# Kernel optimization log

Hardware: AMD Instinct MI355X
Metric: run time of the kernel (lower is better)

Reference implementation:

```python
import jax, jax.numpy as jnp
import numpy as np

N_NODES = 50000
N_EDGES = 800000
IN_C, HID_C, OUT_C = 256, 256, 128


def gcn_conv(x, W, b, row, col, n_nodes):
    """PyG GCNConv: linear transform, symmetric-normalized aggregation, bias.
    row/col already include self-loops. Messages flow row -> col."""
    h = x @ W  # [N, out]
    deg = jax.ops.segment_sum(jnp.ones_like(col, dtype=h.dtype), col, num_segments=n_nodes)
    d_inv_sqrt = jnp.where(deg > 0, jax.lax.rsqrt(jnp.maximum(deg, 1e-12)), 0.0)
    norm = d_inv_sqrt[row] * d_inv_sqrt[col]  # [E]
    msg = h[row] * norm[:, None]              # gather + scale, [E, out]
    out = jax.ops.segment_sum(msg, col, num_segments=n_nodes)  # scatter-add
    return out + b


def setup_inputs() -> dict:
    key = jax.random.key(0)
    k_x, k_e, k_w1, k_w2 = jax.random.split(key, 4)
    x = jax.random.normal(k_x, (N_NODES, IN_C), dtype=jnp.float32)
    edge_index = jax.random.randint(k_e, (2, N_EDGES), 0, N_NODES, dtype=jnp.int64)
    # Glorot-style init for GCN weights, zeros bias (PyG default)
    s1 = float(np.sqrt(6.0 / (IN_C + HID_C)))
    s2 = float(np.sqrt(6.0 / (HID_C + OUT_C)))
    W1 = jax.random.uniform(k_w1, (IN_C, HID_C), dtype=jnp.float32, minval=-s1, maxval=s1)
    b1 = jnp.zeros((HID_C,), dtype=jnp.float32)
    W2 = jax.random.uniform(k_w2, (HID_C, OUT_C), dtype=jnp.float32, minval=-s2, maxval=s2)
    b2 = jnp.zeros((OUT_C,), dtype=jnp.float32)
    return {"x": x, "edge_index": edge_index, "W1": W1, "b1": b1, "W2": W2, "b2": b2}


def reference(x, edge_index, W1, b1, W2, b2):
    n = x.shape[0]
    # add self-loops (PyG GCNConv default add_self_loops=True)
    loops = jnp.arange(n, dtype=edge_index.dtype)
    row = jnp.concatenate([edge_index[0], loops])
    col = jnp.concatenate([edge_index[1], loops])
    h = gcn_conv(x, W1, b1, row, col, n)
    h = jax.nn.relu(h)  # dropout p=0.0 -> identity
    out = gcn_conv(h, W2, b2, row, col, n)
    return out
```

## Files before the change

### kernel.cpp

```cpp
#include <hip/hip_runtime.h>

#define NN 50000
#define NE 800000
#define IN_C 256
#define HID_C 256
#define OUT_C 128

#define NET (NE + NN)
#define NBUCK 196
#define CHUNK 4096
#define NPA 196
#define CAP_B 5120
#define NGRP (NN / 16)

typedef unsigned short u16;
typedef unsigned int u32;
typedef __attribute__((ext_vector_type(8))) short short8;
typedef __attribute__((ext_vector_type(4))) short short4_t;
typedef __attribute__((ext_vector_type(8))) unsigned short ushort8;
typedef __attribute__((ext_vector_type(4))) float f32x4;
typedef __attribute__((ext_vector_type(4))) unsigned u32x4;
typedef __attribute__((ext_vector_type(4), aligned(4))) unsigned u32x4u;

#define CPS ((size_t)(NN + 1) * 32)

__device__ __forceinline__ u16 f2b(float f) {
  unsigned int u = __float_as_uint(f);
  return (u16)((u + 0x7FFFu + ((u >> 16) & 1u)) >> 16);
}
__device__ __forceinline__ float b2f(u16 s) {
  return __uint_as_float(((unsigned int)s) << 16);
}


__global__ __launch_bounds__(256) void convw_zero(const float* __restrict__ W1,
                                                  const float* __restrict__ W2,
                                                  u16* __restrict__ W1t,
                                                  u16* __restrict__ W2t,
                                                  int* __restrict__ cnt,
                                                  u16* __restrict__ Hb,
                                                  int nzb) {
  int b = blockIdx.x;
  if (b < 256) {
    int id = b * 256 + threadIdx.x;
    if (id < 256 * 256) {
      int n = id >> 8, k = id & 255;
      W1t[id] = f2b(W1[k * 256 + n]);
    }
    if (id < 128 * 256) {
      int n = id >> 8, k = id & 255;
      W2t[id] = f2b(W2[k * 128 + n]);
    }
  } else if (b < 256 + nzb) {
    int i = (b - 256) * 256 + threadIdx.x;
    if (i < NN) cnt[i] = 1;
  } else {
    int t = threadIdx.x;
    Hb[(size_t)(t >> 5) * CPS + (size_t)NN * 32 + (t & 31)] = 0;
  }
}


__global__ __launch_bounds__(256) void hist_kernel(const int* __restrict__ col,
                                                   int* __restrict__ cnt, int E) {
  int e = blockIdx.x * blockDim.x + threadIdx.x;
  if (e < E) atomicAdd(&cnt[col[e]], 1);
}

__global__ __launch_bounds__(256) void scan1_kernel(const int* __restrict__ cnt,
                                                    int* __restrict__ bsum, int n) {
  __shared__ int ws[4];
  int i = blockIdx.x * 256 + threadIdx.x;
  int lane = threadIdx.x & 63, wid = threadIdx.x >> 6;
  int v = (i < n) ? cnt[i] : 0;
#pragma unroll
  for (int off = 32; off > 0; off >>= 1) v += __shfl_down(v, off, 64);
  if (lane == 0) ws[wid] = v;
  __syncthreads();
  if (threadIdx.x == 0) bsum[blockIdx.x] = ws[0] + ws[1] + ws[2] + ws[3];
}

__global__ __launch_bounds__(256) void scan2_kernel(const int* __restrict__ bsum,
                                                    int* __restrict__ boff,
                                                    int* __restrict__ row_off,
                                                    int nb, int n) {
  __shared__ int wsum[4], wpre[5];
  int lane = threadIdx.x & 63, wid = threadIdx.x >> 6;
  int v = (threadIdx.x < nb) ? bsum[threadIdx.x] : 0;
  int s = v;
#pragma unroll
  for (int off = 1; off < 64; off <<= 1) {
    int t = __shfl_up(s, off, 64);
    if (lane >= off) s += t;
  }
  if (lane == 63) wsum[wid] = s;
  __syncthreads();
  if (threadIdx.x == 0) {
    int acc = 0;
#pragma unroll
    for (int w = 0; w < 4; ++w) { wpre[w] = acc; acc += wsum[w]; }
    wpre[4] = acc;
  }
  __syncthreads();
  if (threadIdx.x < nb) boff[threadIdx.x] = wpre[wid] + (s - v);
  if (threadIdx.x == 0) row_off[n] = wpre[4];
}

__global__ __launch_bounds__(256) void scan3_kernel(const int* __restrict__ cnt,
                                                    const int* __restrict__ boff,
                                                    int* __restrict__ row_off,
                                                    int* __restrict__ bcur,
                                                    float* __restrict__ dinv, int n) {
  __shared__ int wsum[4], wpre[4];
  int i = blockIdx.x * 256 + threadIdx.x;
  int lane = threadIdx.x & 63, wid = threadIdx.x >> 6;
  int v = (i < n) ? cnt[i] : 0;
  int s = v;
#pragma unroll
  for (int off = 1; off < 64; off <<= 1) {
    int t = __shfl_up(s, off, 64);
    if (lane >= off) s += t;
  }
  if (lane == 63) wsum[wid] = s;
  __syncthreads();
  if (threadIdx.x == 0) {
    int acc = 0;
#pragma unroll
    for (int w = 0; w < 4; ++w) { wpre[w] = acc; acc += wsum[w]; }
  }
  __syncthreads();
  if (i < n) {
    int off = boff[blockIdx.x] + wpre[wid] + (s - v);
    row_off[i] = off;
    if ((i & 255) == 0) bcur[i >> 8] = off;
    dinv[i] = rsqrtf((float)v);
  }
}


template <bool A_IS_F32, bool PLANAR_C>
__device__ __forceinline__ void gemm_body(const void* __restrict__ Ap,
                                          const u16* __restrict__ Bt,
                                          const float* __restrict__ dscale,
                                          u16* __restrict__ C, int M, int N,
                                          int bx, int by,
                                          u16 (&Asl)[2][5120], u16 (&Bsl)[2][5120]) {
  const int tid = threadIdx.x;
  const int row0 = by * 128;
  const int col0 = bx * 128;

  f32x4 acc[4][4] = {};

  const int seg = tid & 7;
  const int rb = tid >> 3;
  const int wave = tid >> 6, lane = tid & 63;
  const int wm = wave >> 1, wn = wave & 1;
  const int qr = lane & 15, quad = lane >> 4;

  float4 aF[4];
  ushort4 aU[4];
  ushort4 bR[4];

  auto load_tiles = [&](int k0) {
    if constexpr (A_IS_F32) {
      const float* A = (const float*)Ap;
#pragma unroll
      for (int i = 0; i < 4; ++i) {
        int gr = row0 + rb + i * 32;
        aF[i] = (gr < M) ? *(const float4*)&A[(size_t)gr * 256 + k0 + seg * 4]
                         : make_float4(0.f, 0.f, 0.f, 0.f);
      }
    } else {
      const u16* A = (const u16*)Ap;
#pragma unroll
      for (int i = 0; i < 4; ++i) {
        int gr = row0 + rb + i * 32;
        aU[i] = (gr < M) ? *(const ushort4*)&A[(size_t)gr * 256 + k0 + seg * 4]
                         : make_ushort4(0, 0, 0, 0);
      }
    }
#pragma unroll
    for (int i = 0; i < 4; ++i) {
      int n = rb + i * 32;
      bR[i] = *(const ushort4*)&Bt[(size_t)(col0 + n) * 256 + k0 + seg * 4];
    }
  };

  auto write_lds = [&](int buf) {
#pragma unroll
    for (int i = 0; i < 4; ++i) {
      int r = rb + i * 32;
      ushort4 u;
      if constexpr (A_IS_F32) {
        u.x = f2b(aF[i].x); u.y = f2b(aF[i].y);
        u.z = f2b(aF[i].z); u.w = f2b(aF[i].w);
      } else {
        u = aU[i];
      }
      *(ushort4*)&Asl[buf][r * 40 + seg * 4] = u;
      *(ushort4*)&Bsl[buf][r * 40 + seg * 4] = bR[i];
    }
  };

  load_tiles(0);
  write_lds(0);
  __syncthreads();

#pragma unroll
  for (int it = 0; it < 8; ++it) {
    const int cur = it & 1;
    if (it < 7) load_tiles((it + 1) * 32);

    short8 afr[4], bfr[4];
#pragma unroll
    for (int mt = 0; mt < 4; ++mt)
      afr[mt] = *(const short8*)&Asl[cur][(wm * 64 + mt * 16 + qr) * 40 + quad * 8];
#pragma unroll
    for (int nt = 0; nt < 4; ++nt)
      bfr[nt] = *(const short8*)&Bsl[cur][(wn * 64 + nt * 16 + qr) * 40 + quad * 8];
#pragma unroll
    for (int mt = 0; mt < 4; ++mt)
#pragma unroll
      for (int nt = 0; nt < 4; ++nt)
        acc[mt][nt] = __builtin_amdgcn_mfma_f32_16x16x32_bf16(afr[mt], bfr[nt], acc[mt][nt], 0, 0, 0);

    if (it < 7) {
      write_lds(1 - cur);
      __syncthreads();
    }
  }

#pragma unroll
  for (int mt = 0; mt < 4; ++mt) {
#pragma unroll
    for (int i = 0; i < 4; ++i) {
      int gr = row0 + wm * 64 + mt * 16 + quad * 4 + i;
      if (gr < M) {
        float sc = dscale[gr];
#pragma unroll
        for (int nt = 0; nt < 4; ++nt) {
          int gc = col0 + wn * 64 + nt * 16 + qr;
          u16 val = f2b(acc[mt][nt][i] * sc);
          if constexpr (PLANAR_C)
            C[(size_t)(gc >> 5) * CPS + (size_t)gr * 32 + (gc & 31)] = val;
          else
            C[(size_t)gr * N + gc] = val;
        }
      }
    }
  }
}

template <bool A_IS_F32, bool PLANAR_C>
__global__ __launch_bounds__(256) void gemm_mfma(const void* __restrict__ Ap,
                                                 const u16* __restrict__ Bt,
                                                 const float* __restrict__ dscale,
                                                 u16* __restrict__ C, int M, int N,
                                                 u16* __restrict__ zrow) {
  if (zrow != nullptr && blockIdx.x == 0 && blockIdx.y == 0 && threadIdx.x < 128) {
    int t = threadIdx.x;
    zrow[(size_t)(t >> 5) * CPS + (size_t)NN * 32 + (t & 31)] = 0;
  }
  __shared__ u16 Asl[2][5120];
  __shared__ u16 Bsl[2][5120];
  gemm_body<A_IS_F32, PLANAR_C>(Ap, Bt, dscale, C, M, N, blockIdx.x, blockIdx.y, Asl, Bsl);
}

__global__ __launch_bounds__(256) void gemm1_scatter(const float* __restrict__ x,
                                                     const u16* __restrict__ W1t,
                                                     const float* __restrict__ dinv,
                                                     u16* __restrict__ Hb, int M, int N,
                                                     int ngb,
                                                     const int* __restrict__ row,
                                                     const int* __restrict__ col,
                                                     int* __restrict__ bcur,
                                                     uint2* __restrict__ stage, int E) {
  __shared__ u16 ABsl[4][5120];
  int b = blockIdx.x;
  if (b < ngb) {
    gemm_body<true, true>(x, W1t, dinv, Hb, M, N, b & 1, b >> 1,
                          *reinterpret_cast<u16(*)[2][5120]>(&ABsl[0]),
                          *reinterpret_cast<u16(*)[2][5120]>(&ABsl[2]));
  } else {
    uint2* pairs = (uint2*)ABsl;
    int* hcnt = (int*)((char*)ABsl + 32768);
    int* hscan = hcnt + 256;
    int* hbase = hscan + 256;
    int* lcur = hbase + 256;

    const int tid = threadIdx.x;
    const int blk = b - ngb;
    const int e0 = blk * CHUNK;

    hcnt[tid] = 0;
    __syncthreads();

    int ecol[16], erow[16];
#pragma unroll
    for (int j = 0; j < 16; ++j) {
      int e = e0 + j * 256 + tid;
      if (e < E) {
        ecol[j] = col[e];
        erow[j] = row[e];
        atomicAdd(&hcnt[ecol[j] >> 8], 1);
      } else {
        ecol[j] = -1;
      }
    }
    __syncthreads();

    hscan[tid] = hcnt[tid];
    __syncthreads();
#pragma unroll
    for (int off = 1; off < 256; off <<= 1) {
      int t = (tid >= off) ? hscan[tid - off] : 0;
      __syncthreads();
      hscan[tid] += t;
      __syncthreads();
    }

    lcur[tid] = 0;
    if (hcnt[tid] > 0) hbase[tid] = atomicAdd(&bcur[tid], hcnt[tid]);
    __syncthreads();

#pragma unroll
    for (int j = 0; j < 16; ++j) {
      if (ecol[j] >= 0) {
        int bk = ecol[j] >> 8;
        int p = atomicAdd(&lcur[bk], 1);
        pairs[(hscan[bk] - hcnt[bk]) + p] = make_uint2((unsigned)erow[j], (unsigned)ecol[j]);
      }
    }
    __syncthreads();

    int mtot = hscan[255];
    for (int s = tid; s < mtot; s += 256) {
      uint2 pr = pairs[s];
      int bk = (int)(pr.y >> 8);
      stage[hbase[bk] + (s - (hscan[bk] - hcnt[bk]))] = pr;
    }
  }
}

__global__ __launch_bounds__(256) void csr_sort(const uint2* __restrict__ stage,
                                                const int* __restrict__ row_off,
                                                u32* __restrict__ csrp) {
  __shared__ int cur[256];
  __shared__ u32 outb[CAP_B];
  const int b = blockIdx.x;
  const int base_node = b << 8;
  const int nnodes = min(256, NN - base_node);
  const int tid = threadIdx.x;
  const int bstart = row_off[base_node];
  const int bend = row_off[min(base_node + 256, NN)];
  if (tid < nnodes) {
    int c0 = row_off[base_node + tid] - bstart;
    outb[c0] = (u32)(base_node + tid) | ((u32)(tid & 15) << 16);
    cur[tid] = c0 + 1;
  }
  __syncthreads();
  const int m = bend - bstart;
  const int mreal = m - nnodes;
  for (int i = tid; i < mreal; i += 256) {
    uint2 pr = stage[bstart + i];
    int cl = ((int)pr.y - base_node) & 255;
    int p = atomicAdd(&cur[cl], 1);
    u32 val = (pr.x & 0xFFFFu) | ((u32)(cl & 15) << 16);
    if (p < CAP_B) outb[p] = val;
    else if (bstart + p < NET) csrp[bstart + p] = val;
  }
  __syncthreads();
  const int mm = min(m, CAP_B);
  for (int i = tid; i < mm; i += 256) csrp[bstart + i] = outb[i];
}

template <int NPL, int OUTC, bool RELU_BF16>
__global__ __launch_bounds__(256) void agg_mfma(const u16* __restrict__ h,
                                                const int* __restrict__ row_off,
                                                const u32* __restrict__ csrp,
                                                const float* __restrict__ dinv,
                                                const float* __restrict__ bias,
                                                void* __restrict__ outp) {
  __shared__ char lds[4][2048];
  const int slice = blockIdx.x % NPL;
  const int wave = threadIdx.x >> 6;
  const int g = (blockIdx.x / NPL) * 4 + wave;
  if (g >= NGRP) return;
  const int lane = threadIdx.x & 63;
  const int qr = lane & 15, quad = lane >> 4;
  const int s = lane >> 1, half = lane & 1;
  const u16* hpl = h + (size_t)slice * CPS;
  const int beg = row_off[g * 16];
  const int end = row_off[g * 16 + 16];
  char* wl = lds[wave];
  char* wp = wl + (half * 1024 + ((s >> 2) & 1) * 512 + (s >> 3) * 128 + (s & 3) * 32);
  const unsigned trb = (unsigned)(size_t)(wl) + (unsigned)(lane * 8);

  f32x4 acc0 = {}, acc1 = {};
  for (int base = beg; base < end; base += 32) {
    int p = base + s;
    unsigned src = (p < end) ? (csrp[p] & 0xFFFFu) : (unsigned)NN;
    const u16* rp = hpl + (size_t)src * 32 + half * 16;
    u32x4 d0 = *(const u32x4*)rp;
    u32x4 d1 = *(const u32x4*)(rp + 8);
    u32x4u w0 = *(const u32x4u*)&csrp[base + quad * 8];
    u32x4u w1 = *(const u32x4u*)&csrp[base + quad * 8 + 4];
    short8 afr;
#pragma unroll
    for (int j = 0; j < 4; ++j) {
      afr[j]     = (short)(((w0[j] >> 16) == (unsigned)qr) ? 0x3F80 : 0);
      afr[j + 4] = (short)(((w1[j] >> 16) == (unsigned)qr) ? 0x3F80 : 0);
    }
    *(u32x4*)wp = d0;
    *(u32x4*)(wp + 16) = d1;
    short4_t t00, t01, t10, t11;
    asm volatile("s_waitcnt lgkmcnt(0)\n\t"
                 "ds_read_b64_tr_b16 %0, %4 offset:0\n\t"
                 "ds_read_b64_tr_b16 %1, %4 offset:512\n\t"
                 "ds_read_b64_tr_b16 %2, %4 offset:1024\n\t"
                 "ds_read_b64_tr_b16 %3, %4 offset:1536\n\t"
                 "s_waitcnt lgkmcnt(0)"
                 : "=&v"(t00), "=&v"(t01), "=&v"(t10), "=&v"(t11)
                 : "v"(trb)
                 : "memory");
    __builtin_amdgcn_sched_barrier(0);
    short8 b0 = __builtin_shufflevector(t00, t01, 0, 1, 2, 3, 4, 5, 6, 7);
    short8 b1 = __builtin_shufflevector(t10, t11, 0, 1, 2, 3, 4, 5, 6, 7);
    acc0 = __builtin_amdgcn_mfma_f32_16x16x32_bf16(afr, b0, acc0, 0, 0, 0);
    acc1 = __builtin_amdgcn_mfma_f32_16x16x32_bf16(afr, b1, acc1, 0, 0, 0);
  }
  const int node0 = g * 16 + quad * 4;
  const int chb = slice * 32;
  float bv0 = bias[chb + qr];
  float bv1 = bias[chb + 16 + qr];
#pragma unroll
  for (int i = 0; i < 4; ++i) {
    float dv = dinv[node0 + i];
    float r0 = acc0[i] * dv + bv0;
    float r1 = acc1[i] * dv + bv1;
    if constexpr (RELU_BF16) {
      u16* o = (u16*)outp;
      o[(size_t)(node0 + i) * OUTC + chb + qr] = f2b(fmaxf(r0, 0.f));
      o[(size_t)(node0 + i) * OUTC + chb + 16 + qr] = f2b(fmaxf(r1, 0.f));
    } else {
      float* o = (float*)outp;
      o[(size_t)(node0 + i) * OUTC + chb + qr] = r0;
      o[(size_t)(node0 + i) * OUTC + chb + 16 + qr] = r1;
    }
  }
}


extern "C" void kernel_launch(void* const* d_in, const int* in_sizes, int n_in,
                              void* d_out, int out_size, void* d_ws, size_t ws_size,
                              hipStream_t stream) {
  const float* x = (const float*)d_in[0];
  const int* ei = (const int*)d_in[1];
  const float* W1 = (const float*)d_in[2];
  const float* b1 = (const float*)d_in[3];
  const float* W2 = (const float*)d_in[4];
  const float* b2 = (const float*)d_in[5];
  float* out = (float*)d_out;

  const int* row = ei;
  const int* col = ei + NE;

  const int NB = (NN + 255) / 256;

  u16* Hb = (u16*)d_ws;
  u16* H2b = Hb + (size_t)(NN + 1) * 256;
  u16* H3b = H2b + (size_t)NN * 256;
  u16* W1t = H3b + (size_t)(NN + 1) * 128;
  u16* W2t = W1t + 256 * 256;
  int* cnt = (int*)(W2t + 128 * 256);
  int* row_off = cnt + NN;
  int* bcur = row_off + NN + 4;
  float* dinv = (float*)(bcur + 256);
  int* bsum = (int*)(dinv + NN);
  int* boff = bsum + 200;
  u32* csrp = (u32*)(boff + 200);
  uint2* stage = (uint2*)H3b;

  convw_zero<<<256 + NB + 1, 256, 0, stream>>>(W1, W2, W1t, W2t, cnt, Hb, NB);
  hist_kernel<<<(NE + 255) / 256, 256, 0, stream>>>(col, cnt, NE);
  scan1_kernel<<<NB, 256, 0, stream>>>(cnt, bsum, NN);
  scan2_kernel<<<1, 256, 0, stream>>>(bsum, boff, row_off, NB, NN);
  scan3_kernel<<<NB, 256, 0, stream>>>(cnt, boff, row_off, bcur, dinv, NN);

  {
    const int ngb = (HID_C / 128) * ((NN + 127) / 128);
    gemm1_scatter<<<ngb + NPA, 256, 0, stream>>>(x, W1t, dinv, Hb, NN, HID_C, ngb,
                                                 row, col, bcur, stage, NE);
  }
  csr_sort<<<NBUCK, 256, 0, stream>>>(stage, row_off, csrp);

  const int NG4 = (NGRP + 3) / 4;
  agg_mfma<8, 256, true><<<NG4 * 8, 256, 0, stream>>>(
      Hb, row_off, csrp, dinv, b1, H2b);

  {
    dim3 grid(OUT_C / 128, (NN + 127) / 128);
    gemm_mfma<false, true><<<grid, 256, 0, stream>>>(H2b, W2t, dinv, H3b, NN, OUT_C, H3b);
  }

  agg_mfma<4, 128, false><<<NG4 * 4, 256, 0, stream>>>(
      H3b, row_off, csrp, dinv, b2, out);
}
```

Baseline: 277.9 us.

## Software-pipeline CSR index and feature gathers in MFMA aggregation loop

After: 328.8 us. 1.18x slower.

```diff
diff --git a/kernel.cpp b/kernel.cpp
--- a/kernel.cpp
+++ b/kernel.cpp
@@ -392,27 +392,41 @@
   const u16* hpl = h + (size_t)slice * CPS;
   const int beg = row_off[g * 16];
   const int end = row_off[g * 16 + 16];
+  const int nsteps = (end - beg + 31) >> 5;
   char* wl = lds[wave];
   char* wp = wl + (half * 1024 + ((s >> 2) & 1) * 512 + (s >> 3) * 128 + (s & 3) * 32);
   const unsigned trb = (unsigned)(size_t)(wl) + (unsigned)(lane * 8);
 
+  auto ldC = [&](int t, u32& cw, u32x4u& w0, u32x4u& w1) {
+    int base = beg + t * 32;
+    cw = __builtin_nontemporal_load(&csrp[base + s]);
+    w0 = __builtin_nontemporal_load((const u32x4u*)&csrp[base + quad * 8]);
+    w1 = __builtin_nontemporal_load((const u32x4u*)&csrp[base + quad * 8 + 4]);
+  };
+  auto ldG = [&](int t, u32 cw, u32x4& d0, u32x4& d1) {
+    int p = beg + t * 32 + s;
+    unsigned src = (p < end) ? (cw & 0xFFFFu) : (unsigned)NN;
+    const u16* rp = hpl + (size_t)src * 32 + half * 16;
+    d0 = *(const u32x4*)rp;
+    d1 = *(const u32x4*)(rp + 8);
+  };
+
+  u32 cw0, cw1, cw2;
+  u32x4u w0a, w1a, w0b, w1b, w0c, w1c;
+  ldC(0, cw0, w0a, w1a);
+  ldC(1, cw1, w0b, w1b);
+  ldC(2, cw2, w0c, w1c);
+  u32x4 gd0, gd1, nd0, nd1;
+  ldG(0, cw0, gd0, gd1);
+
   f32x4 acc0 = {}, acc1 = {};
-  for (int base = beg; base < end; base += 32) {
-    int p = base + s;
-    unsigned src = (p < end) ? (csrp[p] & 0xFFFFu) : (unsigned)NN;
-    const u16* rp = hpl + (size_t)src * 32 + half * 16;
-    u32x4 d0 = *(const u32x4*)rp;
-    u32x4 d1 = *(const u32x4*)(rp + 8);
-    u32x4u w0 = *(const u32x4u*)&csrp[base + quad * 8];
-    u32x4u w1 = *(const u32x4u*)&csrp[base + quad * 8 + 4];
-    short8 afr;
-#pragma unroll
-    for (int j = 0; j < 4; ++j) {
-      afr[j]     = (short)(((w0[j] >> 16) == (unsigned)qr) ? 0x3F80 : 0);
-      afr[j + 4] = (short)(((w1[j] >> 16) == (unsigned)qr) ? 0x3F80 : 0);
-    }
-    *(u32x4*)wp = d0;
-    *(u32x4*)(wp + 16) = d1;
+  for (int t = 0; t < nsteps; ++t) {
+    u32 cw3;
+    u32x4u w0n, w1n;
+    ldC(t + 3, cw3, w0n, w1n);
+    if (t + 1 < nsteps) ldG(t + 1, cw1, nd0, nd1);
+    *(u32x4*)wp = gd0;
+    *(u32x4*)(wp + 16) = gd1;
     short4_t t00, t01, t10, t11;
     asm volatile("s_waitcnt lgkmcnt(0)\n\t"
                  "ds_read_b64_tr_b16 %0, %4 offset:0\n\t"
@@ -424,10 +438,20 @@
                  : "v"(trb)
                  : "memory");
     __builtin_amdgcn_sched_barrier(0);
+    short8 afr;
+#pragma unroll
+    for (int j = 0; j < 4; ++j) {
+      afr[j]     = (short)(((w0a[j] >> 16) == (unsigned)qr) ? 0x3F80 : 0);
+      afr[j + 4] = (short)(((w1a[j] >> 16) == (unsigned)qr) ? 0x3F80 : 0);
+    }
     short8 b0 = __builtin_shufflevector(t00, t01, 0, 1, 2, 3, 4, 5, 6, 7);
     short8 b1 = __builtin_shufflevector(t10, t11, 0, 1, 2, 3, 4, 5, 6, 7);
     acc0 = __builtin_amdgcn_mfma_f32_16x16x32_bf16(afr, b0, acc0, 0, 0, 0);
     acc1 = __builtin_amdgcn_mfma_f32_16x16x32_bf16(afr, b1, acc1, 0, 0, 0);
+    cw0 = cw1; w0a = w0b; w1a = w1b;
+    cw1 = cw2; w0b = w0c; w1b = w1c;
+    cw2 = cw3; w0c = w0n; w1c = w1n;
+    gd0 = nd0; gd1 = nd1;
   }
   const int node0 = g * 16 + quad * 4;
   const int chb = slice * 32;
```

## Replace MFMA one-hot aggregation with direct per-node gather-sum

Applied to the files above, without the earlier changes.

After: 268.1 us. -3.5%, faster.

```diff
diff --git a/kernel.cpp b/kernel.cpp
--- a/kernel.cpp
+++ b/kernel.cpp
@@ -11,14 +11,13 @@
 #define CHUNK 4096
 #define NPA 196
 #define CAP_B 5120
-#define NGRP (NN / 16)
 
 typedef unsigned short u16;
 typedef unsigned int u32;
 typedef __attribute__((ext_vector_type(8))) short short8;
-typedef __attribute__((ext_vector_type(4))) short short4_t;
 typedef __attribute__((ext_vector_type(8))) unsigned short ushort8;
 typedef __attribute__((ext_vector_type(4))) float f32x4;
+typedef __attribute__((ext_vector_type(2))) float f32x2;
 typedef __attribute__((ext_vector_type(4))) unsigned u32x4;
 typedef __attribute__((ext_vector_type(4), aligned(4))) unsigned u32x4u;
 
@@ -355,7 +354,7 @@
   const int bend = row_off[min(base_node + 256, NN)];
   if (tid < nnodes) {
     int c0 = row_off[base_node + tid] - bstart;
-    outb[c0] = (u32)(base_node + tid) | ((u32)(tid & 15) << 16);
+    outb[c0] = (u32)(base_node + tid);
     cur[tid] = c0 + 1;
   }
   __syncthreads();
@@ -365,7 +364,7 @@
     uint2 pr = stage[bstart + i];
     int cl = ((int)pr.y - base_node) & 255;
     int p = atomicAdd(&cur[cl], 1);
-    u32 val = (pr.x & 0xFFFFu) | ((u32)(cl & 15) << 16);
+    u32 val = pr.x & 0xFFFFu;
     if (p < CAP_B) outb[p] = val;
     else if (bstart + p < NET) csrp[bstart + p] = val;
   }
@@ -375,78 +374,80 @@
 }
 
 template <int NPL, int OUTC, bool RELU_BF16>
-__global__ __launch_bounds__(256) void agg_mfma(const u16* __restrict__ h,
-                                                const int* __restrict__ row_off,
-                                                const u32* __restrict__ csrp,
-                                                const float* __restrict__ dinv,
-                                                const float* __restrict__ bias,
-                                                void* __restrict__ outp) {
-  __shared__ char lds[4][2048];
+__global__ __launch_bounds__(256) void agg_gather(const u16* __restrict__ h,
+                                                  const int* __restrict__ row_off,
+                                                  const u32* __restrict__ csrp,
+                                                  const float* __restrict__ dinv,
+                                                  const float* __restrict__ bias,
+                                                  void* __restrict__ outp) {
   const int slice = blockIdx.x % NPL;
   const int wave = threadIdx.x >> 6;
-  const int g = (blockIdx.x / NPL) * 4 + wave;
-  if (g >= NGRP) return;
   const int lane = threadIdx.x & 63;
-  const int qr = lane & 15, quad = lane >> 4;
-  const int s = lane >> 1, half = lane & 1;
+  const int nd = lane >> 2;
+  const int c = lane & 3;
+  const int v = (blockIdx.x / NPL) * 64 + wave * 16 + nd;
+  if (v >= NN) return;
   const u16* hpl = h + (size_t)slice * CPS;
-  const int beg = row_off[g * 16];
-  const int end = row_off[g * 16 + 16];
-  char* wl = lds[wave];
-  char* wp = wl + (half * 1024 + ((s >> 2) & 1) * 512 + (s >> 3) * 128 + (s & 3) * 32);
-  const unsigned trb = (unsigned)(size_t)(wl) + (unsigned)(lane * 8);
-
-  f32x4 acc0 = {}, acc1 = {};
-  for (int base = beg; base < end; base += 32) {
-    int p = base + s;
-    unsigned src = (p < end) ? (csrp[p] & 0xFFFFu) : (unsigned)NN;
-    const u16* rp = hpl + (size_t)src * 32 + half * 16;
-    u32x4 d0 = *(const u32x4*)rp;
-    u32x4 d1 = *(const u32x4*)(rp + 8);
-    u32x4u w0 = *(const u32x4u*)&csrp[base + quad * 8];
-    u32x4u w1 = *(const u32x4u*)&csrp[base + quad * 8 + 4];
-    short8 afr;
-#pragma unroll
-    for (int j = 0; j < 4; ++j) {
-      afr[j]     = (short)(((w0[j] >> 16) == (unsigned)qr) ? 0x3F80 : 0);
-      afr[j + 4] = (short)(((w1[j] >> 16) == (unsigned)qr) ? 0x3F80 : 0);
-    }
-    *(u32x4*)wp = d0;
-    *(u32x4*)(wp + 16) = d1;
-    short4_t t00, t01, t10, t11;
-    asm volatile("s_waitcnt lgkmcnt(0)\n\t"
-                 "ds_read_b64_tr_b16 %0, %4 offset:0\n\t"
-                 "ds_read_b64_tr_b16 %1, %4 offset:512\n\t"
-                 "ds_read_b64_tr_b16 %2, %4 offset:1024\n\t"
-                 "ds_read_b64_tr_b16 %3, %4 offset:1536\n\t"
-                 "s_waitcnt lgkmcnt(0)"
-                 : "=&v"(t00), "=&v"(t01), "=&v"(t10), "=&v"(t11)
-                 : "v"(trb)
-                 : "memory");
-    __builtin_amdgcn_sched_barrier(0);
-    short8 b0 = __builtin_shufflevector(t00, t01, 0, 1, 2, 3, 4, 5, 6, 7);
-    short8 b1 = __builtin_shufflevector(t10, t11, 0, 1, 2, 3, 4, 5, 6, 7);
-    acc0 = __builtin_amdgcn_mfma_f32_16x16x32_bf16(afr, b0, acc0, 0, 0, 0);
-    acc1 = __builtin_amdgcn_mfma_f32_16x16x32_bf16(afr, b1, acc1, 0, 0, 0);
-  }
-  const int node0 = g * 16 + quad * 4;
-  const int chb = slice * 32;
-  float bv0 = bias[chb + qr];
-  float bv1 = bias[chb + 16 + qr];
-#pragma unroll
-  for (int i = 0; i < 4; ++i) {
-    float dv = dinv[node0 + i];
-    float r0 = acc0[i] * dv + bv0;
-    float r1 = acc1[i] * dv + bv1;
-    if constexpr (RELU_BF16) {
-      u16* o = (u16*)outp;
-      o[(size_t)(node0 + i) * OUTC + chb + qr] = f2b(fmaxf(r0, 0.f));
-      o[(size_t)(node0 + i) * OUTC + chb + 16 + qr] = f2b(fmaxf(r1, 0.f));
-    } else {
-      float* o = (float*)outp;
-      o[(size_t)(node0 + i) * OUTC + chb + qr] = r0;
-      o[(size_t)(node0 + i) * OUTC + chb + 16 + qr] = r1;
-    }
+  const int beg = row_off[v], end = row_off[v + 1];
+  const int coff = c * 8;
+
+  f32x2 a0 = {}, a1 = {}, a2 = {}, a3 = {};
+  for (int p = beg; p < end; p += 8) {
+    u32x4u cwa = *(const u32x4u*)&csrp[p];
+    u32x4u cwb = *(const u32x4u*)&csrp[p + 4];
+    unsigned s0 = (p + 0 < end) ? (cwa[0] & 0xFFFFu) : (unsigned)NN;
+    unsigned s1 = (p + 1 < end) ? (cwa[1] & 0xFFFFu) : (unsigned)NN;
+    unsigned s2 = (p + 2 < end) ? (cwa[2] & 0xFFFFu) : (unsigned)NN;
+    unsigned s3 = (p + 3 < end) ? (cwa[3] & 0xFFFFu) : (unsigned)NN;
+    unsigned s4 = (p + 4 < end) ? (cwb[0] & 0xFFFFu) : (unsigned)NN;
+    unsigned s5 = (p + 5 < end) ? (cwb[1] & 0xFFFFu) : (unsigned)NN;
+    unsigned s6 = (p + 6 < end) ? (cwb[2] & 0xFFFFu) : (unsigned)NN;
+    unsigned s7 = (p + 7 < end) ? (cwb[3] & 0xFFFFu) : (unsigned)NN;
+    u32x4 g0 = *(const u32x4*)&hpl[(size_t)s0 * 32 + coff];
+    u32x4 g1 = *(const u32x4*)&hpl[(size_t)s1 * 32 + coff];
+    u32x4 g2 = *(const u32x4*)&hpl[(size_t)s2 * 32 + coff];
+    u32x4 g3 = *(const u32x4*)&hpl[(size_t)s3 * 32 + coff];
+    u32x4 g4 = *(const u32x4*)&hpl[(size_t)s4 * 32 + coff];
+    u32x4 g5 = *(const u32x4*)&hpl[(size_t)s5 * 32 + coff];
+    u32x4 g6 = *(const u32x4*)&hpl[(size_t)s6 * 32 + coff];
+    u32x4 g7 = *(const u32x4*)&hpl[(size_t)s7 * 32 + coff];
+#pragma unroll
+    for (int q = 0; q < 4; ++q) {
+      f32x2 t;
+      f32x2 acc = {};
+      t[0] = __uint_as_float(g0[q] << 16); t[1] = __uint_as_float(g0[q] & 0xffff0000u); acc += t;
+      t[0] = __uint_as_float(g1[q] << 16); t[1] = __uint_as_float(g1[q] & 0xffff0000u); acc += t;
+      t[0] = __uint_as_float(g2[q] << 16); t[1] = __uint_as_float(g2[q] & 0xffff0000u); acc += t;
+      t[0] = __uint_as_float(g3[q] << 16); t[1] = __uint_as_float(g3[q] & 0xffff0000u); acc += t;
+      t[0] = __uint_as_float(g4[q] << 16); t[1] = __uint_as_float(g4[q] & 0xffff0000u); acc += t;
+      t[0] = __uint_as_float(g5[q] << 16); t[1] = __uint_as_float(g5[q] & 0xffff0000u); acc += t;
+      t[0] = __uint_as_float(g6[q] << 16); t[1] = __uint_as_float(g6[q] & 0xffff0000u); acc += t;
+      t[0] = __uint_as_float(g7[q] << 16); t[1] = __uint_as_float(g7[q] & 0xffff0000u); acc += t;
+      if (q == 0) a0 += acc;
+      else if (q == 1) a1 += acc;
+      else if (q == 2) a2 += acc;
+      else a3 += acc;
+    }
+  }
+  float aa[8] = {a0[0], a0[1], a1[0], a1[1], a2[0], a2[1], a3[0], a3[1]};
+  const int cg = slice * 32 + coff;
+  float dv = dinv[v];
+  float4 bv0 = *(const float4*)&bias[cg];
+  float4 bv1 = *(const float4*)&bias[cg + 4];
+  float bb[8] = {bv0.x, bv0.y, bv0.z, bv0.w, bv1.x, bv1.y, bv1.z, bv1.w};
+  if constexpr (RELU_BF16) {
+    u16* o = (u16*)outp;
+    ushort8 ov;
+#pragma unroll
+    for (int i = 0; i < 8; ++i) ov[i] = (short)f2b(fmaxf(aa[i] * dv + bb[i], 0.f));
+    *(ushort8*)&o[(size_t)v * OUTC + cg] = ov;
+  } else {
+    float* o = (float*)outp;
+    float ov[8];
+#pragma unroll
+    for (int i = 0; i < 8; ++i) ov[i] = aa[i] * dv + bb[i];
+    *(float4*)&o[(size_t)v * OUTC + cg] = make_float4(ov[0], ov[1], ov[2], ov[3]);
+    *(float4*)&o[(size_t)v * OUTC + cg + 4] = make_float4(ov[4], ov[5], ov[6], ov[7]);
   }
 }
 
@@ -494,8 +495,8 @@
   }
   csr_sort<<<NBUCK, 256, 0, stream>>>(stage, row_off, csrp);
 
-  const int NG4 = (NGRP + 3) / 4;
-  agg_mfma<8, 256, true><<<NG4 * 8, 256, 0, stream>>>(
+  const int NGB = (NN + 63) / 64;
+  agg_gather<8, 256, true><<<NGB * 8, 256, 0, stream>>>(
       Hb, row_off, csrp, dinv, b1, H2b);
 
   {
@@ -503,6 +504,6 @@
     gemm_mfma<false, true><<<grid, 256, 0, stream>>>(H2b, W2t, dinv, H3b, NN, OUT_C, H3b);
   }
 
-  agg_mfma<4, 128, false><<<NG4 * 4, 256, 0, stream>>>(
+  agg_gather<4, 128, false><<<NGB * 4, 256, 0, stream>>>(
       H3b, row_off, csrp, dinv, b2, out);
 }
```
